# Optimization experiments

Measured on AMD Instinct MI355X. Metric: run time of the kernel, lower is better.

The kernel has to match this reference:

```python
import jax, jax.numpy as jnp
import numpy as np

B, N, F, E, K, R, H = 16, 2048, 2048, 128, 10, 2, 2


def setup_inputs() -> dict:
    key = jax.random.key(0)
    ks = jax.random.split(key, 11)
    s = 0.1  # keep embeddings close so the Gaussian kernel does not underflow
    rel = jax.random.normal(ks[0], (B, E), jnp.float32) * s
    arg1 = jax.random.normal(ks[1], (B, E), jnp.float32) * s
    arg2 = jax.random.normal(ks[2], (B, E), jnp.float32) * s
    fact_rel = jax.random.normal(ks[3], (B, F, E), jnp.float32) * s
    fact_arg1 = jax.random.normal(ks[4], (B, F, E), jnp.float32) * s
    fact_arg2 = jax.random.normal(ks[5], (B, F, E), jnp.float32) * s
    entity_embeddings = jax.random.normal(ks[6], (B, N, E), jnp.float32) * s
    hop_W = jax.random.normal(ks[7], (R, H, E, E), jnp.float32) / jnp.sqrt(jnp.float32(E))
    hop_b = jax.random.normal(ks[8], (R, H, E), jnp.float32) * 0.01
    nb_facts = jax.random.randint(ks[9], (B,), F // 2, F + 1, jnp.int32)
    nb_entities = jax.random.randint(ks[10], (B,), N // 2, N + 1, jnp.int32)
    return dict(rel=rel, arg1=arg1, arg2=arg2, fact_rel=fact_rel,
                fact_arg1=fact_arg1, fact_arg2=fact_arg2,
                entity_embeddings=entity_embeddings, hop_W=hop_W, hop_b=hop_b,
                nb_facts=nb_facts, nb_entities=nb_entities)


def reference(rel, arg1, arg2, fact_rel, fact_arg1, fact_arg2,
              entity_embeddings, hop_W, hop_b, nb_facts, nb_entities):
    # Gaussian kernel k(x,y) = exp(-||x-y||^2 / 2), batched: x [B,T,E], y [B,F,E] -> [B,T,F]
    def kern(x, y):
        d2 = (jnp.sum(x * x, -1)[:, :, None] + jnp.sum(y * y, -1)[:, None, :]
              - 2.0 * jnp.einsum('bte,bfe->btf', x, y))
        return jnp.exp(-0.5 * d2)

    fact_mask = (jnp.arange(F) < nb_facts[:, None])[:, None, :]            # [B,1,F]
    ent_mask = (jnp.arange(N) < nb_entities[:, None]).astype(rel.dtype)    # [B,N]

    # BatchNeuralKB.score: max over (valid) facts of product of kernels. [B,T,E]x3 -> [B,T]
    def model_score(r, a1, a2):
        s = kern(r, fact_rel) * kern(a1, fact_arg1) * kern(a2, fact_arg2)  # [B,T,F]
        return jnp.max(jnp.where(fact_mask, s, 0.0), axis=-1)

    # BatchNeuralKB.forward, (s,p,?) -> score per candidate object entity. [B,1,E] -> [B,N]
    def forward_sp(r, a1):
        kr = jnp.where(fact_mask, kern(r, fact_rel) * kern(a1, fact_arg1), 0.0)  # [B,1,F]
        kE = kern(entity_embeddings, fact_arg2)                                  # [B,N,F]
        return jnp.max(kr * kE, axis=-1) * ent_mask                              # [B,N]

    # (?,p,o) -> score per candidate subject entity
    def forward_po(r, a2):
        kr = jnp.where(fact_mask, kern(r, fact_rel) * kern(a2, fact_arg2), 0.0)
        kE = kern(entity_embeddings, fact_arg1)
        return jnp.max(kr * kE, axis=-1) * ent_mask

    # r_score(depth=1) = max(depth_r_score(0), depth_r_score(1))
    # depth_r_score(0) == model.score
    scores_0 = model_score(rel[:, None], arg1[:, None], arg2[:, None])[:, 0]  # [B]

    global_res = None
    for r_idx in range(R):
        is_rev = (r_idx % 2 == 1)
        # LinearReformulator: hop relations from rel
        h1 = rel @ hop_W[r_idx, 0] + hop_b[r_idx, 0]  # [B,E]
        h2 = rel @ hop_W[r_idx, 1] + hop_b[r_idx, 1]
        # hop 1: r_hop -> scores over all entities, then top-k beam
        if is_rev:
            sp = forward_po(h1[:, None], arg1[:, None])  # [B,N]
        else:
            sp = forward_sp(h1[:, None], arg1[:, None])
        z_scores, z_idx = jax.lax.top_k(sp, K)                                  # [B,K]
        z_emb = jnp.take_along_axis(entity_embeddings, z_idx[:, :, None], axis=1)  # [B,K,E]
        # final hop: r_score(depth=0) == model.score with branched args
        h2k = jnp.broadcast_to(h2[:, None, :], (B, K, E))
        a2k = jnp.broadcast_to(arg2[:, None, :], (B, K, E))
        if is_rev:
            s2 = model_score(h2k, a2k, z_emb)  # [B,K]
        else:
            s2 = model_score(h2k, z_emb, a2k)
        rule_scores = jnp.minimum(s2, z_scores)   # tnorm = 'min'
        rule_res = jnp.max(rule_scores, axis=1)   # max over branches [B]
        global_res = rule_res if global_res is None else jnp.maximum(global_res, rule_res)

    return jnp.maximum(scores_0, global_res)
```

## Files before the change

### kernel.cpp

```cpp
#include <hip/hip_runtime.h>
#include <math.h>

#define Bb 16
#define Nn 2048
#define Ff 2048
#define Ee 128
#define Kk 10
#define S2FC 8
#define S2F (Ff / S2FC)

typedef __attribute__((ext_vector_type(8))) short short8;
typedef __attribute__((ext_vector_type(4))) float f32x4;
typedef unsigned int u32;

__device__ inline float wave_sum(float x) {
    for (int o = 32; o; o >>= 1) x += __shfl_down(x, o);
    return x;
}

__device__ inline void bsplit(float x, unsigned short& h, unsigned short& l) {
    unsigned int u = __float_as_uint(x);
    h = (unsigned short)(u >> 16);
    float hf = __uint_as_float(u & 0xFFFF0000u);
    l = (unsigned short)(__float_as_uint(x - hf) >> 16);
}

__device__ inline void atomic_fmax_pos(float* addr, float v) {
    atomicMax((unsigned int*)addr, __float_as_uint(v));
}

__device__ inline void gload_lds16(const void* g, void* l) {
    __builtin_amdgcn_global_load_lds(
        (const __attribute__((address_space(1))) u32*)g,
        (__attribute__((address_space(3))) u32*)l, 16, 0, 0);
}


__global__ __launch_bounds__(256) void k_pfe(
    const float* __restrict__ rel, const float* __restrict__ arg1,
    const float* __restrict__ arg2, const float* __restrict__ frel,
    const float* __restrict__ fa1, const float* __restrict__ fa2,
    const float* __restrict__ ent, const float* __restrict__ hop_W,
    const float* __restrict__ hop_b, const int* __restrict__ nb_facts,
    unsigned short* __restrict__ B0, unsigned short* __restrict__ B1,
    float* __restrict__ ent_norm, float* __restrict__ c0, float* __restrict__ c1,
    float* __restrict__ s2b0, float* __restrict__ s2b1,
    float* __restrict__ sp0, float* __restrict__ sp1, float* __restrict__ out) {
    int bx = blockIdx.x;
    int tid = threadIdx.x;
    if (bx < 256) {
        int fcb = bx & 15, b = bx >> 4;
        int nbf = nb_facts[b];
        const float NI = -INFINITY;
        int fbase = fcb * 128;
        if (fbase >= nbf) {
            if (tid < 128) {
                size_t o = (size_t)b * Ff + fbase + tid;
                c0[o] = NI; c1[o] = NI; s2b0[o] = NI; s2b1[o] = NI;
            }
            return;
        }
        __shared__ float q[7][Ee];
        __shared__ float rows[128][129];
        __shared__ float bred[4];
        if (tid < 128) {
            q[0][tid] = rel[b * Ee + tid];
            q[1][tid] = arg1[b * Ee + tid];
            q[2][tid] = arg2[b * Ee + tid];
        }
        __syncthreads();
        {
            int e = tid & 127, hf = tid >> 7;
            const float* W0 = hop_W + (size_t)(hf * 2) * Ee * Ee;
            const float* W1 = W0 + (size_t)Ee * Ee;
            float a0 = hop_b[(hf * 2) * Ee + e];
            float a1 = hop_b[(hf * 2 + 1) * Ee + e];
#pragma unroll 8
            for (int qq = 0; qq < Ee; ++qq) {
                float rq = q[0][qq];
                a0 += rq * W0[qq * Ee + e];
                a1 += rq * W1[qq * Ee + e];
            }
            q[3 + hf][e] = a0;
            q[5 + hf][e] = a1;
        }

        __syncthreads();
        for (int idx = tid; idx < 128 * 32; idx += 256) {
            int row = idx >> 5, c4 = (idx & 31) * 4;
            float4 v = *(const float4*)(frel + ((size_t)b * Ff + fbase + row) * Ee + c4);
            rows[row][c4] = v.x; rows[row][c4 + 1] = v.y;
            rows[row][c4 + 2] = v.z; rows[row][c4 + 3] = v.w;
        }
        __syncthreads();
        float d_rr = 0, d_h10 = 0, d_h11 = 0, d_h20 = 0, d_h21 = 0;
        if (tid < 128) {
#pragma unroll 8
            for (int e = 0; e < Ee; ++e) {
                float fr = rows[tid][e], t;
                t = q[0][e] - fr; d_rr  += t * t;
                t = q[3][e] - fr; d_h10 += t * t;
                t = q[4][e] - fr; d_h11 += t * t;
                t = q[5][e] - fr; d_h20 += t * t;
                t = q[6][e] - fr; d_h21 += t * t;
            }
        }
        __syncthreads();
        for (int idx = tid; idx < 128 * 32; idx += 256) {
            int row = idx >> 5, c4 = (idx & 31) * 4;
            float4 v = *(const float4*)(fa1 + ((size_t)b * Ff + fbase + row) * Ee + c4);
            rows[row][c4] = v.x; rows[row][c4 + 1] = v.y;
            rows[row][c4 + 2] = v.z; rows[row][c4 + 3] = v.w;
        }
        __syncthreads();
        float d_a11 = 0, d_a21 = 0, n1 = 0;
        if (tid < 128) {
#pragma unroll 8
            for (int e = 0; e < Ee; ++e) {
                float f1 = rows[tid][e], t;
                t = q[1][e] - f1; d_a11 += t * t;
                t = q[2][e] - f1; d_a21 += t * t;
                n1 += f1 * f1;
            }
        }
        __syncthreads();
        for (int idx = tid; idx < 128 * 32; idx += 256) {
            int row = idx >> 5, c4 = (idx & 31) * 4;
            float4 v = *(const float4*)(fa2 + ((size_t)b * Ff + fbase + row) * Ee + c4);
            rows[row][c4] = v.x; rows[row][c4 + 1] = v.y;
            rows[row][c4 + 2] = v.z; rows[row][c4 + 3] = v.w;
        }
        __syncthreads();
        float d_a22 = 0, d_a12 = 0, n2 = 0;
        if (tid < 128) {
#pragma unroll 8
            for (int e = 0; e < Ee; ++e) {
                float f2 = rows[tid][e], t;
                t = q[2][e] - f2; d_a22 += t * t;
                t = q[1][e] - f2; d_a12 += t * t;
                n2 += f2 * f2;
            }
        }

        bool valid = (tid < 128) && (fbase + tid < nbf);
        if (tid < 128) {
            size_t o = (size_t)b * Ff + fbase + tid;
            c0[o]   = valid ? (-0.5f * (d_h10 + d_a11 + n2)) : NI;
            c1[o]   = valid ? (-0.5f * (d_h11 + d_a12 + n1)) : NI;
            s2b0[o] = valid ? (-0.5f * (d_h20 + d_a22)) : NI;
            s2b1[o] = valid ? (-0.5f * (d_h21 + d_a21)) : NI;
        }
        float lsc = valid ? (-0.5f * (d_rr + d_a11 + d_a22)) : NI;
        for (int m = 32; m; m >>= 1) lsc = fmaxf(lsc, __shfl_down(lsc, m));
        if ((tid & 63) == 0) bred[tid >> 6] = lsc;
        __syncthreads();
        if (tid == 0) {
            float m = fmaxf(fmaxf(bred[0], bred[1]), fmaxf(bred[2], bred[3]));
            atomic_fmax_pos(out + b, expf(m));
        }
    } else if (bx < 256 + 4096) {
        __shared__ uint4 tlds[16 * 33];
        int bxx = bx - 256;
        int y = bxx >> 11, bxi = bxx & 2047;
        int oct = tid & 15, fl = tid >> 4;
        int b = bxi >> 7, fbase = (bxi & 127) * 16;
        const float* src = (y == 0) ? fa2 : fa1;
        const float* s = src + ((size_t)b * Ff + fbase + fl) * Ee + oct * 8;
        float4 v0 = *(const float4*)s;
        float4 v1 = *(const float4*)(s + 4);
        float xs[8] = {v0.x, v0.y, v0.z, v0.w, v1.x, v1.y, v1.z, v1.w};
        unsigned short hi[8], lo[8];
#pragma unroll
        for (int j = 0; j < 8; ++j) bsplit(xs[j], hi[j], lo[j]);
        uint4 ph, pl;
        ph.x = (unsigned)hi[0] | ((unsigned)hi[1] << 16);
        ph.y = (unsigned)hi[2] | ((unsigned)hi[3] << 16);
        ph.z = (unsigned)hi[4] | ((unsigned)hi[5] << 16);
        ph.w = (unsigned)hi[6] | ((unsigned)hi[7] << 16);
        pl.x = (unsigned)lo[0] | ((unsigned)lo[1] << 16);
        pl.y = (unsigned)lo[2] | ((unsigned)lo[3] << 16);
        pl.z = (unsigned)lo[4] | ((unsigned)lo[5] << 16);
        pl.w = (unsigned)lo[6] | ((unsigned)lo[7] << 16);
        tlds[fl * 33 + oct * 2]     = ph;
        tlds[fl * 33 + oct * 2 + 1] = pl;
        __syncthreads();
        int F4 = (fbase >> 4) & 1, F5 = (fbase >> 5) & 1;
        unsigned char* ob = (unsigned char*)((y == 0) ? B0 : B1) +
                            (((size_t)b << 20) + (size_t)(fbase >> 6) * 32768 +
                             F5 * 1024 + F4 * 512);
#pragma unroll
        for (int uu = 0; uu < 2; ++uu) {
            int u = tid + uu * 256;
            int o = u >> 5, sS = u & 31;
            int s0 = sS & 1, s1 = (sS >> 1) & 1, s2 = (sS >> 2) & 1;
            int s3 = (sS >> 3) & 1, s4 = (sS >> 4) & 1;
            int part = s0 ^ s3;
            int fll = (s1 ^ s4) | ((s2 ^ F4) << 1) | (s3 << 2) | (s4 << 3);
            *(uint4*)(ob + o * 2048 + sS * 16) = tlds[fll * 33 + o * 2 + part];
        }
    } else {
        int row  = (bx - (256 + 4096)) * 4 + (tid >> 6);
        int lane = tid & 63;
        const float* p = ent + (size_t)row * Ee;
        float a = p[lane], c = p[lane + 64];
        float s = wave_sum(a * a + c * c);
        if (lane == 0) {
            ent_norm[row] = s;
            sp0[row] = 0.0f;
            sp1[row] = 0.0f;
        }
    }
}

#define BMs 256

__global__ __launch_bounds__(512, 2) void k_spmax_mfma(
    const float* __restrict__ ent, const unsigned short* __restrict__ B0,
    const unsigned short* __restrict__ B1, const float* __restrict__ c0,
    const float* __restrict__ c1, const float* __restrict__ ent_norm,
    const int* __restrict__ nb_facts, const int* __restrict__ nb_entities,
    float* __restrict__ sp0, float* __restrict__ sp1) {
    int bid = blockIdx.x;
    int br = bid & 31, nblk = bid >> 5;
    int b = br >> 1, r = br & 1;
    const unsigned short* Bt = (r == 0) ? B0 : B1;
    const float* cb = ((r == 0) ? c0 : c1) + (size_t)b * Ff;
    float* sp = ((r == 0) ? sp0 : sp1) + (size_t)b * Nn;

    int tid = threadIdx.x;
    int ne = nb_entities[b];
    if (nblk * BMs >= ne) return;
    int nch = (nb_facts[b] + 63) >> 6;

    __shared__ uint4 ldsB4[2 * 2048];

    int wave = tid >> 6, lane = tid & 63;
    int wm = wave >> 1, wn = wave & 1;
    int lane15 = lane & 15, quad = lane >> 4;

    short8 ah[4][4], al[4][4];
    {
        const float* abase = ent + ((size_t)b * Nn + (size_t)nblk * BMs + wm * 64) * Ee;
#pragma unroll
        for (int i = 0; i < 4; ++i)
#pragma unroll
            for (int ks = 0; ks < 4; ++ks) {
                const float* p = abase + (size_t)(i * 16 + lane15) * Ee + ks * 32 + quad * 8;
                float4 v0 = *(const float4*)p;
                float4 v1 = *(const float4*)(p + 4);
                float xs[8] = {v0.x, v0.y, v0.z, v0.w, v1.x, v1.y, v1.z, v1.w};
                short8 hi8, lo8;
#pragma unroll
                for (int j = 0; j < 8; ++j) {
                    unsigned short hh, ll;
                    bsplit(xs[j], hh, ll);
                    hi8[j] = (short)hh;
                    lo8[j] = (short)ll;
                }
                ah[i][ks] = hi8;
                al[i][ks] = lo8;
            }
    }

    int offA = (wn * 32 + lane15) * 32;
    int physA0 = offA ^ (((offA >> 7) & 7) << 4);
    int offB = offA + 512;
    int physB0 = offB ^ (((offB >> 7) & 7) << 4);
    int qoff = quad * 2048;

    unsigned char* ldsB = (unsigned char*)ldsB4;
    const unsigned char* gB = (const unsigned char*)Bt + ((size_t)b << 20);

#pragma unroll
    for (int t = 0; t < 4; ++t) {
        int seg = t * 8 + wave;
        gload_lds16(gB + seg * 1024 + lane * 16, ldsB + seg * 1024);
    }
    __syncthreads();

    float mmax[4][4];
#pragma unroll
    for (int i = 0; i < 4; ++i)
#pragma unroll
        for (int rr = 0; rr < 4; ++rr) mmax[i][rr] = -INFINITY;

    int cur = 0;
    for (int c = 0; c < nch; ++c) {
        if (c + 1 < nch) {
            const unsigned char* gc = gB + (size_t)(c + 1) * 32768;
            unsigned char* lb = ldsB + (cur ^ 1) * 32768;
#pragma unroll
            for (int t = 0; t < 4; ++t) {
                int seg = t * 8 + wave;
                gload_lds16(gc + seg * 1024 + lane * 16, lb + seg * 1024);
            }
        }
        float cj0 = cb[c * 64 + wn * 32 + lane15];
        float cj1 = cb[c * 64 + wn * 32 + 16 + lane15];
        f32x4 acc[4][2];
#pragma unroll
        for (int i = 0; i < 4; ++i) {
            acc[i][0] = (f32x4){cj0, cj0, cj0, cj0};
            acc[i][1] = (f32x4){cj1, cj1, cj1, cj1};
        }
        const unsigned char* bb = ldsB + cur * 32768;
#pragma unroll
        for (int ks = 0; ks < 4; ++ks) {
            const unsigned char* bk = bb + ks * 8192 + qoff;
            short8 bh0 = *(const short8*)(bk + physA0);
            short8 bl0 = *(const short8*)(bk + (physA0 ^ 16));
            short8 bh1 = *(const short8*)(bk + physB0);
            short8 bl1 = *(const short8*)(bk + (physB0 ^ 16));
#pragma unroll
            for (int i = 0; i < 4; ++i) {
                acc[i][0] = __builtin_amdgcn_mfma_f32_16x16x32_bf16(ah[i][ks], bh0, acc[i][0], 0, 0, 0);
                acc[i][0] = __builtin_amdgcn_mfma_f32_16x16x32_bf16(al[i][ks], bh0, acc[i][0], 0, 0, 0);
                acc[i][0] = __builtin_amdgcn_mfma_f32_16x16x32_bf16(ah[i][ks], bl0, acc[i][0], 0, 0, 0);
                acc[i][1] = __builtin_amdgcn_mfma_f32_16x16x32_bf16(ah[i][ks], bh1, acc[i][1], 0, 0, 0);
                acc[i][1] = __builtin_amdgcn_mfma_f32_16x16x32_bf16(al[i][ks], bh1, acc[i][1], 0, 0, 0);
                acc[i][1] = __builtin_amdgcn_mfma_f32_16x16x32_bf16(ah[i][ks], bl1, acc[i][1], 0, 0, 0);
            }
        }

#pragma unroll
        for (int j = 0; j < 2; ++j)
#pragma unroll
            for (int i = 0; i < 4; ++i)
#pragma unroll
                for (int rr = 0; rr < 4; ++rr)
                    mmax[i][rr] = fmaxf(mmax[i][rr], acc[i][j][rr]);

        __syncthreads();
        cur ^= 1;
    }

    float* red = (float*)ldsB;
#pragma unroll
    for (int i = 0; i < 4; ++i)
#pragma unroll
        for (int rr = 0; rr < 4; ++rr) {
            float v = mmax[i][rr];
#pragma unroll
            for (int m = 1; m < 16; m <<= 1) v = fmaxf(v, __shfl_xor(v, m));
            if (lane15 == 0) red[(wm * 64 + i * 16 + quad * 4 + rr) * 2 + wn] = v;
        }
    __syncthreads();
    if (tid < BMs) {
        float m = fmaxf(red[tid * 2], red[tid * 2 + 1]);
        int n = nblk * BMs + tid;
        if (n < ne)
            sp[n] = expf(m - 0.5f * ent_norm[(size_t)b * Nn + n]);
    }
}

__global__ __launch_bounds__(256) void k_s2t(
    const float* __restrict__ ent, const float* __restrict__ fa1,
    const float* __restrict__ fa2, const float* __restrict__ s2b0,
    const float* __restrict__ s2b1, const float* __restrict__ sp0,
    const float* __restrict__ sp1, const int* __restrict__ nb_facts,
    float* __restrict__ out) {
    int fc = blockIdx.x, b = blockIdx.y, r = blockIdx.z;
    if (fc * S2F >= nb_facts[b]) return;
    const float* factX = (r == 0) ? fa1 : fa2;
    const float* s2b   = ((r == 0) ? s2b0 : s2b1) + (size_t)b * Ff;
    const float* sp    = ((r == 0) ? sp0 : sp1) + (size_t)b * Nn;

    __shared__ float zsc[Kk];
    __shared__ int   zidx[Kk];
    __shared__ float zsh[Kk][Ee];
    __shared__ float znorm[Kk];
    __shared__ float red[4][Kk];
    __shared__ float rules[Kk];

    int tid = threadIdx.x;
    int wv = tid >> 6, lane = tid & 63;

    if (wv == 0) {
        float v[Nn / 64];
#pragma unroll
        for (int i = 0; i < Nn / 64; ++i) v[i] = sp[i * 64 + lane];
        for (int k = 0; k < Kk; ++k) {
            float best = -INFINITY; int bidx = 0;
#pragma unroll
            for (int i = 0; i < Nn / 64; ++i)
                if (v[i] > best) { best = v[i]; bidx = i * 64 + lane; }
#pragma unroll
            for (int m = 1; m < 64; m <<= 1) {
                float ov = __shfl_xor(best, m);
                int oi = __shfl_xor(bidx, m);
                if (ov > best || (ov == best && oi < bidx)) { best = ov; bidx = oi; }
            }
            if (lane == 0) { zsc[k] = best; zidx[k] = bidx; }
            if ((bidx & 63) == lane) {
                int slot = bidx >> 6;
#pragma unroll
                for (int i = 0; i < Nn / 64; ++i)
                    if (i == slot) v[i] = -INFINITY;
            }
        }
    }
    __syncthreads();
    for (int idx = tid; idx < Kk * Ee; idx += 256) {
        int k = idx >> 7, e = idx & 127;
        zsh[k][e] = ent[((size_t)b * Nn + zidx[k]) * Ee + e];
    }
    __syncthreads();
    if (tid < Kk) {
        float s = 0.f;
        for (int e = 0; e < Ee; ++e) { float v = zsh[tid][e]; s += v * v; }
        znorm[tid] = s;
    }
    __syncthreads();

    int f = fc * S2F + tid;
    const float* fp = factX + ((size_t)b * Ff + f) * Ee;
    float acc[Kk];
#pragma unroll
    for (int k = 0; k < Kk; ++k) acc[k] = 0.f;
    float nf = 0.f;
#pragma unroll 4
    for (int e0 = 0; e0 < Ee; e0 += 4) {
        float4 v = *(const float4*)(fp + e0);
        nf += v.x * v.x + v.y * v.y + v.z * v.z + v.w * v.w;
#pragma unroll
        for (int k = 0; k < Kk; ++k) {
            float4 z = *(const float4*)&zsh[k][e0];
            acc[k] += z.x * v.x + z.y * v.y + z.z * v.z + z.w * v.w;
        }
    }
    float base = s2b[f] - 0.5f * nf;
    float sc[Kk];
#pragma unroll
    for (int k = 0; k < Kk; ++k) sc[k] = base + acc[k] - 0.5f * znorm[k];
    for (int o = 32; o; o >>= 1)
#pragma unroll
        for (int k = 0; k < Kk; ++k) sc[k] = fmaxf(sc[k], __shfl_down(sc[k], o));
    if ((tid & 63) == 0)
#pragma unroll
        for (int k = 0; k < Kk; ++k) red[wv][k] = sc[k];
    __syncthreads();
    if (tid < Kk) {
        float m = fmaxf(fmaxf(red[0][tid], red[1][tid]), fmaxf(red[2][tid], red[3][tid]));
        rules[tid] = fminf(expf(m), zsc[tid]);
    }
    __syncthreads();
    if (tid == 0) {
        float g = rules[0];
#pragma unroll
        for (int k = 1; k < Kk; ++k) g = fmaxf(g, rules[k]);
        atomic_fmax_pos(out + b, g);
    }
}

extern "C" void kernel_launch(void* const* d_in, const int* in_sizes, int n_in,
                              void* d_out, int out_size, void* d_ws, size_t ws_size,
                              hipStream_t stream) {
    const float* rel  = (const float*)d_in[0];
    const float* arg1 = (const float*)d_in[1];
    const float* arg2 = (const float*)d_in[2];
    const float* frel = (const float*)d_in[3];
    const float* fa1  = (const float*)d_in[4];
    const float* fa2  = (const float*)d_in[5];
    const float* ent  = (const float*)d_in[6];
    const float* hopW = (const float*)d_in[7];
    const float* hopb = (const float*)d_in[8];
    const int* nb_facts    = (const int*)d_in[9];
    const int* nb_entities = (const int*)d_in[10];
    float* out = (float*)d_out;

    float* ws = (float*)d_ws;
    size_t off = 0;
    float* c0       = ws + off; off += (size_t)Bb * Ff;
    float* c1       = ws + off; off += (size_t)Bb * Ff;
    float* s2b0     = ws + off; off += (size_t)Bb * Ff;
    float* s2b1     = ws + off; off += (size_t)Bb * Ff;
    float* sp0      = ws + off; off += (size_t)Bb * Nn;
    float* sp1      = ws + off; off += (size_t)Bb * Nn;
    float* ent_norm = ws + off; off += (size_t)Bb * Nn;
    off = (off + 7) & ~(size_t)7;
    unsigned short* B0 = (unsigned short*)(ws + off); off += (size_t)Bb * 16 * Ff * 8;
    unsigned short* B1 = (unsigned short*)(ws + off); off += (size_t)Bb * 16 * Ff * 8;

    hipMemsetAsync(d_out, 0, (size_t)out_size * sizeof(float), stream);
    k_pfe<<<dim3(256 + 4096 + Bb * Nn / 4), 256, 0, stream>>>(
        rel, arg1, arg2, frel, fa1, fa2, ent, hopW, hopb, nb_facts,
        B0, B1, ent_norm, c0, c1, s2b0, s2b1, sp0, sp1, out);
    k_spmax_mfma<<<dim3(32 * 8), 512, 0, stream>>>(ent, B0, B1, c0, c1, ent_norm,
                                                   nb_facts, nb_entities, sp0, sp1);
    k_s2t<<<dim3(S2FC, Bb, 2), 256, 0, stream>>>(ent, fa1, fa2, s2b0, s2b1,
                                                 sp0, sp1, nb_facts, out);
}
```

Before: 226.5 us.

## Split spmax fact chunks into two halves with atomic work-stealing queue

Result: slower. 240.6 us (+6.2%).

```diff
diff --git a/kernel.cpp b/kernel.cpp
--- a/kernel.cpp
+++ b/kernel.cpp
@@ -219,48 +219,14 @@
     const unsigned short* __restrict__ B1, const float* __restrict__ c0,
     const float* __restrict__ c1, const float* __restrict__ ent_norm,
     const int* __restrict__ nb_facts, const int* __restrict__ nb_entities,
-    float* __restrict__ sp0, float* __restrict__ sp1) {
-    int bid = blockIdx.x;
-    int br = bid & 31, nblk = bid >> 5;
-    int b = br >> 1, r = br & 1;
-    const unsigned short* Bt = (r == 0) ? B0 : B1;
-    const float* cb = ((r == 0) ? c0 : c1) + (size_t)b * Ff;
-    float* sp = ((r == 0) ? sp0 : sp1) + (size_t)b * Nn;
+    float* __restrict__ sp0, float* __restrict__ sp1, int* __restrict__ wcnt) {
+    __shared__ uint4 ldsB4[2 * 2048];
+    __shared__ int ldsItem;
 
     int tid = threadIdx.x;
-    int ne = nb_entities[b];
-    if (nblk * BMs >= ne) return;
-    int nch = (nb_facts[b] + 63) >> 6;
-
-    __shared__ uint4 ldsB4[2 * 2048];
-
     int wave = tid >> 6, lane = tid & 63;
     int wm = wave >> 1, wn = wave & 1;
     int lane15 = lane & 15, quad = lane >> 4;
-
-    short8 ah[4][4], al[4][4];
-    {
-        const float* abase = ent + ((size_t)b * Nn + (size_t)nblk * BMs + wm * 64) * Ee;
-#pragma unroll
-        for (int i = 0; i < 4; ++i)
-#pragma unroll
-            for (int ks = 0; ks < 4; ++ks) {
-                const float* p = abase + (size_t)(i * 16 + lane15) * Ee + ks * 32 + quad * 8;
-                float4 v0 = *(const float4*)p;
-                float4 v1 = *(const float4*)(p + 4);
-                float xs[8] = {v0.x, v0.y, v0.z, v0.w, v1.x, v1.y, v1.z, v1.w};
-                short8 hi8, lo8;
-#pragma unroll
-                for (int j = 0; j < 8; ++j) {
-                    unsigned short hh, ll;
-                    bsplit(xs[j], hh, ll);
-                    hi8[j] = (short)hh;
-                    lo8[j] = (short)ll;
-                }
-                ah[i][ks] = hi8;
-                al[i][ks] = lo8;
-            }
-    }
 
     int offA = (wn * 32 + lane15) * 32;
     int physA0 = offA ^ (((offA >> 7) & 7) << 4);
@@ -269,87 +235,131 @@
     int qoff = quad * 2048;
 
     unsigned char* ldsB = (unsigned char*)ldsB4;
-    const unsigned char* gB = (const unsigned char*)Bt + ((size_t)b << 20);
-
-#pragma unroll
-    for (int t = 0; t < 4; ++t) {
-        int seg = t * 8 + wave;
-        gload_lds16(gB + seg * 1024 + lane * 16, ldsB + seg * 1024);
-    }
-    __syncthreads();
-
-    float mmax[4][4];
-#pragma unroll
-    for (int i = 0; i < 4; ++i)
-#pragma unroll
-        for (int rr = 0; rr < 4; ++rr) mmax[i][rr] = -INFINITY;
-
-    int cur = 0;
-    for (int c = 0; c < nch; ++c) {
-        if (c + 1 < nch) {
-            const unsigned char* gc = gB + (size_t)(c + 1) * 32768;
-            unsigned char* lb = ldsB + (cur ^ 1) * 32768;
-#pragma unroll
-            for (int t = 0; t < 4; ++t) {
-                int seg = t * 8 + wave;
-                gload_lds16(gc + seg * 1024 + lane * 16, lb + seg * 1024);
-            }
-        }
-        float cj0 = cb[c * 64 + wn * 32 + lane15];
-        float cj1 = cb[c * 64 + wn * 32 + 16 + lane15];
-        f32x4 acc[4][2];
-#pragma unroll
-        for (int i = 0; i < 4; ++i) {
-            acc[i][0] = (f32x4){cj0, cj0, cj0, cj0};
-            acc[i][1] = (f32x4){cj1, cj1, cj1, cj1};
-        }
-        const unsigned char* bb = ldsB + cur * 32768;
-#pragma unroll
-        for (int ks = 0; ks < 4; ++ks) {
-            const unsigned char* bk = bb + ks * 8192 + qoff;
-            short8 bh0 = *(const short8*)(bk + physA0);
-            short8 bl0 = *(const short8*)(bk + (physA0 ^ 16));
-            short8 bh1 = *(const short8*)(bk + physB0);
-            short8 bl1 = *(const short8*)(bk + (physB0 ^ 16));
+
+    for (;;) {
+        __syncthreads();
+        if (tid == 0) ldsItem = atomicAdd(wcnt, 1);
+        __syncthreads();
+        int it = ldsItem;
+        if (it >= 512) break;
+        int s = it >> 1, h = it & 1;
+        int br = s & 31, nblk = s >> 5;
+        int b = br >> 1, r = br & 1;
+        int ne = nb_entities[b];
+        if (nblk * BMs >= ne) continue;
+        int nch = (nb_facts[b] + 63) >> 6;
+        if (h >= nch) continue;
+        const unsigned short* Bt = (r == 0) ? B0 : B1;
+        const float* cb = ((r == 0) ? c0 : c1) + (size_t)b * Ff;
+        float* sp = ((r == 0) ? sp0 : sp1) + (size_t)b * Nn;
+        const unsigned char* gB = (const unsigned char*)Bt + ((size_t)b << 20);
+
+        short8 ah[4][4], al[4][4];
+        {
+            const float* abase = ent + ((size_t)b * Nn + (size_t)nblk * BMs + wm * 64) * Ee;
+#pragma unroll
+            for (int i = 0; i < 4; ++i)
+#pragma unroll
+                for (int ks = 0; ks < 4; ++ks) {
+                    const float* p = abase + (size_t)(i * 16 + lane15) * Ee + ks * 32 + quad * 8;
+                    float4 v0 = *(const float4*)p;
+                    float4 v1 = *(const float4*)(p + 4);
+                    float xs[8] = {v0.x, v0.y, v0.z, v0.w, v1.x, v1.y, v1.z, v1.w};
+                    short8 hi8, lo8;
+#pragma unroll
+                    for (int j = 0; j < 8; ++j) {
+                        unsigned short hh, ll;
+                        bsplit(xs[j], hh, ll);
+                        hi8[j] = (short)hh;
+                        lo8[j] = (short)ll;
+                    }
+                    ah[i][ks] = hi8;
+                    al[i][ks] = lo8;
+                }
+        }
+
+#pragma unroll
+        for (int t = 0; t < 4; ++t) {
+            int seg = t * 8 + wave;
+            gload_lds16(gB + (size_t)h * 32768 + seg * 1024 + lane * 16, ldsB + seg * 1024);
+        }
+        __syncthreads();
+
+        float mmax[4][4];
+#pragma unroll
+        for (int i = 0; i < 4; ++i)
+#pragma unroll
+            for (int rr = 0; rr < 4; ++rr) mmax[i][rr] = -INFINITY;
+
+        int nt = (nch - h + 1) >> 1;
+        int cur = 0;
+        for (int t2 = 0; t2 < nt; ++t2) {
+            int c = h + 2 * t2;
+            if (t2 + 1 < nt) {
+                const unsigned char* gc = gB + (size_t)(c + 2) * 32768;
+                unsigned char* lb = ldsB + (cur ^ 1) * 32768;
+#pragma unroll
+                for (int t = 0; t < 4; ++t) {
+                    int seg = t * 8 + wave;
+                    gload_lds16(gc + seg * 1024 + lane * 16, lb + seg * 1024);
+                }
+            }
+            float cj0 = cb[c * 64 + wn * 32 + lane15];
+            float cj1 = cb[c * 64 + wn * 32 + 16 + lane15];
+            f32x4 acc[4][2];
 #pragma unroll
             for (int i = 0; i < 4; ++i) {
-                acc[i][0] = __builtin_amdgcn_mfma_f32_16x16x32_bf16(ah[i][ks], bh0, acc[i][0], 0, 0, 0);
-                acc[i][0] = __builtin_amdgcn_mfma_f32_16x16x32_bf16(al[i][ks], bh0, acc[i][0], 0, 0, 0);
-                acc[i][0] = __builtin_amdgcn_mfma_f32_16x16x32_bf16(ah[i][ks], bl0, acc[i][0], 0, 0, 0);
-                acc[i][1] = __builtin_amdgcn_mfma_f32_16x16x32_bf16(ah[i][ks], bh1, acc[i][1], 0, 0, 0);
-                acc[i][1] = __builtin_amdgcn_mfma_f32_16x16x32_bf16(al[i][ks], bh1, acc[i][1], 0, 0, 0);
-                acc[i][1] = __builtin_amdgcn_mfma_f32_16x16x32_bf16(ah[i][ks], bl1, acc[i][1], 0, 0, 0);
-            }
-        }
-
-#pragma unroll
-        for (int j = 0; j < 2; ++j)
-#pragma unroll
-            for (int i = 0; i < 4; ++i)
-#pragma unroll
-                for (int rr = 0; rr < 4; ++rr)
-                    mmax[i][rr] = fmaxf(mmax[i][rr], acc[i][j][rr]);
-
-        __syncthreads();
-        cur ^= 1;
-    }
-
-    float* red = (float*)ldsB;
-#pragma unroll
-    for (int i = 0; i < 4; ++i)
-#pragma unroll
-        for (int rr = 0; rr < 4; ++rr) {
-            float v = mmax[i][rr];
-#pragma unroll
-            for (int m = 1; m < 16; m <<= 1) v = fmaxf(v, __shfl_xor(v, m));
-            if (lane15 == 0) red[(wm * 64 + i * 16 + quad * 4 + rr) * 2 + wn] = v;
-        }
-    __syncthreads();
-    if (tid < BMs) {
-        float m = fmaxf(red[tid * 2], red[tid * 2 + 1]);
-        int n = nblk * BMs + tid;
-        if (n < ne)
-            sp[n] = expf(m - 0.5f * ent_norm[(size_t)b * Nn + n]);
+                acc[i][0] = (f32x4){cj0, cj0, cj0, cj0};
+                acc[i][1] = (f32x4){cj1, cj1, cj1, cj1};
+            }
+            const unsigned char* bb = ldsB + cur * 32768;
+#pragma unroll
+            for (int ks = 0; ks < 4; ++ks) {
+                const unsigned char* bk = bb + ks * 8192 + qoff;
+                short8 bh0 = *(const short8*)(bk + physA0);
+                short8 bl0 = *(const short8*)(bk + (physA0 ^ 16));
+                short8 bh1 = *(const short8*)(bk + physB0);
+                short8 bl1 = *(const short8*)(bk + (physB0 ^ 16));
+#pragma unroll
+                for (int i = 0; i < 4; ++i) {
+                    acc[i][0] = __builtin_amdgcn_mfma_f32_16x16x32_bf16(ah[i][ks], bh0, acc[i][0], 0, 0, 0);
+                    acc[i][0] = __builtin_amdgcn_mfma_f32_16x16x32_bf16(al[i][ks], bh0, acc[i][0], 0, 0, 0);
+                    acc[i][0] = __builtin_amdgcn_mfma_f32_16x16x32_bf16(ah[i][ks], bl0, acc[i][0], 0, 0, 0);
+                    acc[i][1] = __builtin_amdgcn_mfma_f32_16x16x32_bf16(ah[i][ks], bh1, acc[i][1], 0, 0, 0);
+                    acc[i][1] = __builtin_amdgcn_mfma_f32_16x16x32_bf16(al[i][ks], bh1, acc[i][1], 0, 0, 0);
+                    acc[i][1] = __builtin_amdgcn_mfma_f32_16x16x32_bf16(ah[i][ks], bl1, acc[i][1], 0, 0, 0);
+                }
+            }
+
+#pragma unroll
+            for (int j = 0; j < 2; ++j)
+#pragma unroll
+                for (int i = 0; i < 4; ++i)
+#pragma unroll
+                    for (int rr = 0; rr < 4; ++rr)
+                        mmax[i][rr] = fmaxf(mmax[i][rr], acc[i][j][rr]);
+
+            __syncthreads();
+            cur ^= 1;
+        }
+
+        float* red = (float*)ldsB;
+#pragma unroll
+        for (int i = 0; i < 4; ++i)
+#pragma unroll
+            for (int rr = 0; rr < 4; ++rr) {
+                float v = mmax[i][rr];
+#pragma unroll
+                for (int m = 1; m < 16; m <<= 1) v = fmaxf(v, __shfl_xor(v, m));
+                if (lane15 == 0) red[(wm * 64 + i * 16 + quad * 4 + rr) * 2 + wn] = v;
+            }
+        __syncthreads();
+        if (tid < BMs) {
+            float m = fmaxf(red[tid * 2], red[tid * 2 + 1]);
+            int n = nblk * BMs + tid;
+            if (n < ne)
+                atomic_fmax_pos(&sp[n], expf(m - 0.5f * ent_norm[(size_t)b * Nn + n]));
+        }
     }
 }
 
@@ -477,16 +487,18 @@
     float* sp0      = ws + off; off += (size_t)Bb * Nn;
     float* sp1      = ws + off; off += (size_t)Bb * Nn;
     float* ent_norm = ws + off; off += (size_t)Bb * Nn;
+    int*   wcnt     = (int*)(ws + off); off += 8;
     off = (off + 7) & ~(size_t)7;
     unsigned short* B0 = (unsigned short*)(ws + off); off += (size_t)Bb * 16 * Ff * 8;
     unsigned short* B1 = (unsigned short*)(ws + off); off += (size_t)Bb * 16 * Ff * 8;
 
     hipMemsetAsync(d_out, 0, (size_t)out_size * sizeof(float), stream);
+    hipMemsetAsync(wcnt, 0, sizeof(int), stream);
     k_pfe<<<dim3(256 + 4096 + Bb * Nn / 4), 256, 0, stream>>>(
         rel, arg1, arg2, frel, fa1, fa2, ent, hopW, hopb, nb_facts,
         B0, B1, ent_norm, c0, c1, s2b0, s2b1, sp0, sp1, out);
-    k_spmax_mfma<<<dim3(32 * 8), 512, 0, stream>>>(ent, B0, B1, c0, c1, ent_norm,
-                                                   nb_facts, nb_entities, sp0, sp1);
+    k_spmax_mfma<<<dim3(256), 512, 0, stream>>>(ent, B0, B1, c0, c1, ent_norm,
+                                                nb_facts, nb_entities, sp0, sp1, wcnt);
     k_s2t<<<dim3(S2FC, Bb, 2), 256, 0, stream>>>(ent, fa1, fa2, s2b0, s2b1,
                                                  sp0, sp1, nb_facts, out);
 }
```
